# Kernel optimization log

Measured on AMD Instinct MI355X. Metric: run time of the kernel, lower is better.

The kernel has to match this reference:

```python
import jax, jax.numpy as jnp
import numpy as np

DT = 1.0
V_LAMBDA = 1e-4
V_RIDGE = 1e-4


def third_order_D(Np):
    # [Np-3, Np] banded third-difference operator
    M = Np - 3
    r = jnp.arange(M)
    D = jnp.zeros((M, Np), dtype=jnp.float32)
    D = D.at[r, r].set(-1.0).at[r, r + 1].set(3.0).at[r, r + 2].set(-3.0).at[r, r + 3].set(1.0)
    return D


def setup_inputs() -> dict:
    key = jax.random.key(0)
    k1, k2, k3 = jax.random.split(key, 3)
    B, N = 8192, 64
    dxy = jax.random.normal(k1, (B, N, 2), dtype=jnp.float32)
    theta = jax.random.normal(k2, (B, N + 1), dtype=jnp.float32)
    v0 = jax.random.normal(k3, (B,), dtype=jnp.float32)
    return {"dxy": dxy, "theta": theta, "v0": v0}


def reference(dxy, theta, v0):
    B, N, _ = dxy.shape  # theta: [B, N+1]
    g = (2.0 / DT) * dxy                     # [B, N, 2]
    b = g.reshape(B, 2 * N)                  # interleaved (x, y) per step
    cos_t = jnp.cos(theta)
    sin_t = jnp.sin(theta)

    # Assemble banded data matrix A: [B, 2N, N+1]
    rows = jnp.arange(N)
    A = jnp.zeros((B, 2 * N, N + 1), dtype=dxy.dtype)
    A = A.at[:, 2 * rows, rows].set(cos_t[:, :-1])
    A = A.at[:, 2 * rows, rows + 1].set(cos_t[:, 1:])
    A = A.at[:, 2 * rows + 1, rows].set(sin_t[:, :-1])
    A = A.at[:, 2 * rows + 1, rows + 1].set(sin_t[:, 1:])
    # data weights w = 1 -> Aw == A

    ATA = jnp.einsum('bij,bik->bjk', A, A)           # [B, N+1, N+1]
    rhs = jnp.einsum('bij,bi->bj', A[:, :, 1:], b)   # [B, N]
    rhs = rhs - ATA[:, 1:, 0] * v0[:, None]

    # Smoothness prior: third-order difference, lam3 = v_lambda / dt^6
    D3 = third_order_D(N + 1)
    DTD = (V_LAMBDA / DT ** 6) * (D3.T @ D3)         # [N+1, N+1], shared across batch
    rhs = rhs - DTD[1:, 0] * v0[:, None]

    lhs = ATA[:, 1:, 1:] + DTD[1:, 1:] + V_RIDGE * jnp.eye(N, dtype=dxy.dtype)
    L = jnp.linalg.cholesky(lhs)
    y = jax.scipy.linalg.cho_solve((L, True), rhs[..., None])[..., 0]  # [B, N]
    return jnp.concatenate([v0[:, None], y], axis=-1)                  # [B, N+1]
```

## Files before the change

kernel.cpp:

```cpp
#include <hip/hip_runtime.h>
#include <math.h>

#define LAM3  1e-4f
#define RIDGE 1e-4f
#define NN    64
#define NP    65

__device__ __forceinline__ float d3_diag(int f) {
    if (f == 0 || f == 64) return 1.f;
    if (f == 1 || f == 63) return 10.f;
    if (f == 2 || f == 62) return 19.f;
    return 20.f;
}
__device__ __forceinline__ float d3_off1(int f) {
    if (f == 1 || f == 64) return -3.f;
    if (f == 2 || f == 63) return -12.f;
    return -15.f;
}
__device__ __forceinline__ float d3_off2(int f) {
    if (f == 2 || f == 64) return 3.f;
    return 6.f;
}

__global__ __launch_bounds__(64, 1) void alpamayo_banded_solve(
    const float* __restrict__ dxy,
    const float* __restrict__ theta,
    const float* __restrict__ v0,
    float* __restrict__ out,
    int B)
{
    __shared__ float4 Lrec[NN][64];

    const int tid = threadIdx.x;
    const int b = blockIdx.x * 64 + tid;
    if (b >= B) return;

    const float* th = theta + (long)b * NP;
    const float4* dx4 = (const float4*)(dxy + (long)b * (2 * NN));
    const float v0b = v0[b];

    float dxf[2 * NN];
    #pragma unroll
    for (int j = 0; j < 32; ++j) {
        const float4 q = dx4[j];
        dxf[4 * j + 0] = q.x; dxf[4 * j + 1] = q.y;
        dxf[4 * j + 2] = q.z; dxf[4 * j + 3] = q.w;
    }
    float thr[NP];
    #pragma unroll
    for (int f = 0; f < NP; ++f) thr[f] = th[f];

    float* outp = out + (long)b * NP;
    outp[0] = v0b;

    float z[NN];
    float cp, sp;
    __sincosf(thr[0], &sp, &cp);
    float xc = dxf[0], yc = dxf[1];

    float p1L1 = 0.f, p1L2 = 0.f, p2L1 = 0.f;
    float rd1 = 0.f, rd2 = 0.f, rd3 = 0.f;
    float z1 = 0.f, z2 = 0.f, z3 = 0.f;

    #pragma unroll
    for (int i = 0; i < NN; ++i) {
        const int f = i + 1;
        float cf, sf;
        __sincosf(thr[f], &sf, &cf);
        const float e  = cf * cp + sf * sp;
        const float xs = (f < NN) ? dxf[2 * f]     : 0.f;
        const float ys = (f < NN) ? dxf[2 * f + 1] : 0.f;
        float rr = 2.f * (cf * (xc + xs) + sf * (yc + ys));
        if (i == 0) rr -= (e + LAM3 * -3.f) * v0b;
        if (i == 1) rr -= (LAM3 *  3.f) * v0b;
        if (i == 2) rr -= (LAM3 * -1.f) * v0b;

        const float a0 = (f == NN ? 1.f : 2.f) + LAM3 * d3_diag(f) + RIDGE;
        const float a1 = e + LAM3 * d3_off1(f);
        const float a2 = LAM3 * d3_off2(f);

        const float Li3 = (-LAM3) * rd3;
        const float Li2 = (a2 - Li3 * p2L1) * rd2;
        const float Li1 = (a1 - Li3 * p1L2 - Li2 * p1L1) * rd1;
        const float dg  = a0 - Li3 * Li3 - Li2 * Li2 - Li1 * Li1;
        const float rd0 = __builtin_amdgcn_rsqf(dg);
        const float zi  = (rr - Li3 * z3 - Li2 * z2 - Li1 * z1) * rd0;

        Lrec[i][tid] = make_float4(Li1, Li2, Li3, rd0);
        z[i] = zi;

        p2L1 = p1L1; p1L1 = Li1; p1L2 = Li2;
        rd3 = rd2; rd2 = rd1; rd1 = rd0;
        z3 = z2; z2 = z1; z1 = zi;
        cp = cf; sp = sf; xc = xs; yc = ys;
    }

    float r1L1 = 0.f, r1L2 = 0.f, r1L3 = 0.f;
    float r2L2 = 0.f, r2L3 = 0.f;
    float r3L3 = 0.f;
    float y1 = 0.f, y2 = 0.f, y3 = 0.f;

    #pragma unroll
    for (int i = NN - 1; i >= 0; --i) {
        const float4 rec = Lrec[i][tid];
        const float yi = (z[i] - r1L1 * y1 - r2L2 * y2 - r3L3 * y3) * rec.w;
        outp[1 + i] = yi;
        r3L3 = r2L3; r2L3 = r1L3; r2L2 = r1L2;
        r1L1 = rec.x; r1L2 = rec.y; r1L3 = rec.z;
        y3 = y2; y2 = y1; y1 = yi;
    }
}

extern "C" void kernel_launch(void* const* d_in, const int* in_sizes, int n_in,
                              void* d_out, int out_size, void* d_ws, size_t ws_size,
                              hipStream_t stream) {
    const float* dxy   = (const float*)d_in[0];
    const float* theta = (const float*)d_in[1];
    const float* v0    = (const float*)d_in[2];
    float* out = (float*)d_out;
    const int B = in_sizes[2];
    const int blocks = (B + 63) / 64;
    alpamayo_banded_solve<<<blocks, 64, 0, stream>>>(dxy, theta, v0, out, B);
}
```

Baseline: 64.32 us.

## Stream inputs in 8-step blocks with prefetch and store z in shared memory

Replaces full upfront register loads of theta and dxy with an 8-iteration blocked loop that prefetches the next block's inputs while computing the current block. z is now stored in the shared-memory record instead of a register array, and Li3 is recomputed from rd rather than stored. Out-of-range threads are clamped instead of returning. This is meant to cut register pressure and expose load latency to overlap with compute, at the cost of a non-unrolled loop with runtime boundary branches.

```diff
diff --git a/kernel.cpp b/kernel.cpp
--- a/kernel.cpp
+++ b/kernel.cpp
@@ -6,21 +6,65 @@
 #define NN    64
 #define NP    65
 
-__device__ __forceinline__ float d3_diag(int f) {
-    if (f == 0 || f == 64) return 1.f;
-    if (f == 1 || f == 63) return 10.f;
-    if (f == 2 || f == 62) return 19.f;
-    return 20.f;
-}
-__device__ __forceinline__ float d3_off1(int f) {
-    if (f == 1 || f == 64) return -3.f;
-    if (f == 2 || f == 63) return -12.f;
-    return -15.f;
-}
-__device__ __forceinline__ float d3_off2(int f) {
-    if (f == 2 || f == 64) return 3.f;
-    return 6.f;
-}
+
+#define LOADB(bn_) do {                                                    \
+    const int fb = 8 * (bn_) + 1;                                          \
+    tn0 = thp[fb + 0]; tn1 = thp[fb + 1]; tn2 = thp[fb + 2];               \
+    tn3 = thp[fb + 3]; tn4 = thp[fb + 4]; tn5 = thp[fb + 5];               \
+    tn6 = thp[fb + 6]; tn7 = thp[fb + 7];                                  \
+    const int cb = 16 * (bn_) + 2;                                         \
+    dn0 = *(const float2*)(dxp + cb +  0);                                 \
+    dn1 = *(const float2*)(dxp + cb +  2);                                 \
+    dn2 = *(const float2*)(dxp + cb +  4);                                 \
+    dn3 = *(const float2*)(dxp + cb +  6);                                 \
+    dn4 = *(const float2*)(dxp + cb +  8);                                 \
+    dn5 = *(const float2*)(dxp + cb + 10);                                 \
+    dn6 = *(const float2*)(dxp + cb + 12);                                 \
+    const int c7 = (cb + 14 <= 126) ? (cb + 14) : 126;                     \
+    dn7 = *(const float2*)(dxp + c7);                                      \
+} while (0)
+
+#define FWD(J, TC, DC) do {                                                \
+    float cf, sf; __sincosf((TC), &sf, &cf);                               \
+    const float e = cf * cp + sf * sp;                                     \
+    float xs = (DC).x, ys = (DC).y;                                        \
+    if ((J) == 7) { if (bi == 7) { xs = 0.f; ys = 0.f; } }      \
+    float rr = 2.f * (cf * (xc + xs) + sf * (yc + ys));                    \
+    if ((J) == 0) { if (bi == 0) rr -= (e - 3.f * LAM3) * v0b; }           \
+    if ((J) == 1) { if (bi == 0) rr -= ( 3.f * LAM3) * v0b; }              \
+    if ((J) == 2) { if (bi == 0) rr -= (-LAM3) * v0b; }                    \
+    float dv = 20.f, o1 = -15.f, o2v = 6.f, base0 = 2.f;                   \
+    if ((J) == 0) { if (bi == 0) { dv = 10.f; o1 = -3.f; } }               \
+    if ((J) == 1) { if (bi == 0) { dv = 19.f; o1 = -12.f; o2v = 3.f; } }   \
+    if ((J) == 5) { if (bi == 7) { dv = 19.f; } }                          \
+    if ((J) == 6) { if (bi == 7) { dv = 10.f; o1 = -12.f; } }              \
+    if ((J) == 7) { if (bi == 7) { dv = 1.f; o1 = -3.f; o2v = 3.f;         \
+                                   base0 = 1.f; } }                        \
+    const float a0 = base0 + LAM3 * dv + RIDGE;                            \
+    const float a1 = e + LAM3 * o1;                                        \
+    const float a2 = LAM3 * o2v;                                           \
+    const float Li3 = (-LAM3) * rd3;                  \
+    const float Li2 = (a2 - Li3 * p2L1) * rd2;        \
+    const float Li1 = (a1 - Li3 * p1L2 - Li2 * p1L1) * rd1;                \
+    const float dgv = a0 - Li3 * Li3 - Li2 * Li2 - Li1 * Li1;              \
+    const float rd0 = __builtin_amdgcn_rsqf(dgv);                          \
+    const float zi  = (rr - Li3 * z3 - Li2 * z2 - Li1 * z1) * rd0;         \
+    Lrec[8 * bi + (J)][tid] = make_float4(Li1, Li2, rd0, zi);              \
+    p2L1 = p1L1; p1L1 = Li1; p1L2 = Li2;                                   \
+    rd3 = rd2; rd2 = rd1; rd1 = rd0;                                       \
+    z3 = z2; z2 = z1; z1 = zi;                                             \
+    cp = cf; sp = sf; xc = xs; yc = ys;                                    \
+} while (0)
+
+#define BCK(J, Q) do {                                                     \
+    const float t0 = (Q).w - l1c * y1;                                     \
+    const float t1 = t0 - l2c2 * y2;                                       \
+    const float t2 = t1 + LAM3 * (Q).z * y3;                               \
+    const float yi = t2 * (Q).z;                                           \
+    outp[1 + 8 * bi + (J)] = yi;                                           \
+    l1c = (Q).x; l2c2 = l2c1; l2c1 = (Q).y;                                \
+    y3 = y2; y2 = y1; y1 = yi;                                             \
+} while (0)
 
 __global__ __launch_bounds__(64, 1) void alpamayo_banded_solve(
     const float* __restrict__ dxy,
@@ -32,82 +76,56 @@
     __shared__ float4 Lrec[NN][64];
 
     const int tid = threadIdx.x;
-    const int b = blockIdx.x * 64 + tid;
-    if (b >= B) return;
+    int b = blockIdx.x * 64 + tid;
+    if (b >= B) b = B - 1;
 
-    const float* th = theta + (long)b * NP;
-    const float4* dx4 = (const float4*)(dxy + (long)b * (2 * NN));
+    const float*  thp = theta + (long)b * NP;
+    const float*  dxp = dxy   + (long)b * (2 * NN);
+    float*       outp = out   + (long)b * NP;
     const float v0b = v0[b];
 
-    float dxf[2 * NN];
-    #pragma unroll
-    for (int j = 0; j < 32; ++j) {
-        const float4 q = dx4[j];
-        dxf[4 * j + 0] = q.x; dxf[4 * j + 1] = q.y;
-        dxf[4 * j + 2] = q.z; dxf[4 * j + 3] = q.w;
-    }
-    float thr[NP];
-    #pragma unroll
-    for (int f = 0; f < NP; ++f) thr[f] = th[f];
-
-    float* outp = out + (long)b * NP;
+    float  tn0, tn1, tn2, tn3, tn4, tn5, tn6, tn7;
+    float2 dn0, dn1, dn2, dn3, dn4, dn5, dn6, dn7;
+    LOADB(0);
+    float cp, sp;
+    __sincosf(thp[0], &sp, &cp);
+    float xc, yc;
+    { const float2 d0 = *(const float2*)(dxp); xc = d0.x; yc = d0.y; }
     outp[0] = v0b;
-
-    float z[NN];
-    float cp, sp;
-    __sincosf(thr[0], &sp, &cp);
-    float xc = dxf[0], yc = dxf[1];
 
     float p1L1 = 0.f, p1L2 = 0.f, p2L1 = 0.f;
     float rd1 = 0.f, rd2 = 0.f, rd3 = 0.f;
     float z1 = 0.f, z2 = 0.f, z3 = 0.f;
 
-    #pragma unroll
-    for (int i = 0; i < NN; ++i) {
-        const int f = i + 1;
-        float cf, sf;
-        __sincosf(thr[f], &sf, &cf);
-        const float e  = cf * cp + sf * sp;
-        const float xs = (f < NN) ? dxf[2 * f]     : 0.f;
-        const float ys = (f < NN) ? dxf[2 * f + 1] : 0.f;
-        float rr = 2.f * (cf * (xc + xs) + sf * (yc + ys));
-        if (i == 0) rr -= (e + LAM3 * -3.f) * v0b;
-        if (i == 1) rr -= (LAM3 *  3.f) * v0b;
-        if (i == 2) rr -= (LAM3 * -1.f) * v0b;
+    #pragma unroll 1
+    for (int bi = 0; bi < 8; ++bi) {
+        const float  tc0 = tn0, tc1 = tn1, tc2 = tn2, tc3 = tn3;
+        const float  tc4 = tn4, tc5 = tn5, tc6 = tn6, tc7 = tn7;
+        const float2 dc0 = dn0, dc1 = dn1, dc2 = dn2, dc3 = dn3;
+        const float2 dc4 = dn4, dc5 = dn5, dc6 = dn6, dc7 = dn7;
+        const int bn = (bi < 7) ? bi + 1 : 7;
+        LOADB(bn);
 
-        const float a0 = (f == NN ? 1.f : 2.f) + LAM3 * d3_diag(f) + RIDGE;
-        const float a1 = e + LAM3 * d3_off1(f);
-        const float a2 = LAM3 * d3_off2(f);
-
-        const float Li3 = (-LAM3) * rd3;
-        const float Li2 = (a2 - Li3 * p2L1) * rd2;
-        const float Li1 = (a1 - Li3 * p1L2 - Li2 * p1L1) * rd1;
-        const float dg  = a0 - Li3 * Li3 - Li2 * Li2 - Li1 * Li1;
-        const float rd0 = __builtin_amdgcn_rsqf(dg);
-        const float zi  = (rr - Li3 * z3 - Li2 * z2 - Li1 * z1) * rd0;
-
-        Lrec[i][tid] = make_float4(Li1, Li2, Li3, rd0);
-        z[i] = zi;
-
-        p2L1 = p1L1; p1L1 = Li1; p1L2 = Li2;
-        rd3 = rd2; rd2 = rd1; rd1 = rd0;
-        z3 = z2; z2 = z1; z1 = zi;
-        cp = cf; sp = sf; xc = xs; yc = ys;
+        FWD(0, tc0, dc0); FWD(1, tc1, dc1); FWD(2, tc2, dc2); FWD(3, tc3, dc3);
+        FWD(4, tc4, dc4); FWD(5, tc5, dc5); FWD(6, tc6, dc6); FWD(7, tc7, dc7);
     }
 
-    float r1L1 = 0.f, r1L2 = 0.f, r1L3 = 0.f;
-    float r2L2 = 0.f, r2L3 = 0.f;
-    float r3L3 = 0.f;
+    float l1c = 0.f, l2c1 = 0.f, l2c2 = 0.f;
     float y1 = 0.f, y2 = 0.f, y3 = 0.f;
 
-    #pragma unroll
-    for (int i = NN - 1; i >= 0; --i) {
-        const float4 rec = Lrec[i][tid];
-        const float yi = (z[i] - r1L1 * y1 - r2L2 * y2 - r3L3 * y3) * rec.w;
-        outp[1 + i] = yi;
-        r3L3 = r2L3; r2L3 = r1L3; r2L2 = r1L2;
-        r1L1 = rec.x; r1L2 = rec.y; r1L3 = rec.z;
-        y3 = y2; y2 = y1; y1 = yi;
+    #pragma unroll 1
+    for (int bi = 7; bi >= 0; --bi) {
+        const float4 q7 = Lrec[8 * bi + 7][tid];
+        const float4 q6 = Lrec[8 * bi + 6][tid];
+        const float4 q5 = Lrec[8 * bi + 5][tid];
+        const float4 q4 = Lrec[8 * bi + 4][tid];
+        const float4 q3 = Lrec[8 * bi + 3][tid];
+        const float4 q2 = Lrec[8 * bi + 2][tid];
+        const float4 q1 = Lrec[8 * bi + 1][tid];
+        const float4 q0 = Lrec[8 * bi + 0][tid];
+
+        BCK(7, q7); BCK(6, q6); BCK(5, q5); BCK(4, q4);
+        BCK(3, q3); BCK(2, q2); BCK(1, q1); BCK(0, q0);
     }
 }
 
```

New measurement: 66.65 us. 3.6% more time.
